# Performance work log

Hardware: AMD Instinct MI355X
Metric: run time of the kernel (lower is better)

## Reference

```python
import jax, jax.numpy as jnp
import numpy as np
import math

N_CELLS = 16384
INPUT_DIM = 512
HIDDEN = 512


def build_neighbors(n):
    n_bits = max(1, int(math.ceil(math.log2(n))))
    idx = np.arange(n)
    flips = [idx ^ (1 << b) for b in range(n_bits)]
    ring = [(idx + 1) % n, (idx - 1) % n]
    allnb = np.stack(flips + ring, axis=1)
    # dedupe per row; for power-of-2 n every row has exactly n_bits+1 uniques
    rows = [sorted(set(r.tolist())) for r in allnb]
    return np.asarray(rows, dtype=np.int32)


def setup_inputs() -> dict:
    key = jax.random.key(0)
    ks = jax.random.split(key, 12)
    n, d, h = N_CELLS, INPUT_DIM, HIDDEN
    amp = jax.random.uniform(ks[0], (n, h)) * 0.5 + 0.5
    phase = jax.random.normal(ks[1], (n, h)) * 0.3 + (2 * math.pi * jnp.arange(n) / n)[:, None]
    return {
        "x": jax.random.normal(ks[2], (1, d), dtype=jnp.float32),
        "pump_W": jax.random.normal(ks[3], (n, d), dtype=jnp.float32) / np.sqrt(d),
        "pump_b": jax.random.normal(ks[4], (n,), dtype=jnp.float32) * 0.01,
        "dec_W": jax.random.normal(ks[5], (d, 2 * h), dtype=jnp.float32) / np.sqrt(2 * h),
        "dec_b": jax.random.normal(ks[6], (d,), dtype=jnp.float32) * 0.01,
        "cs_re": (amp * jnp.cos(phase)).astype(jnp.float32),
        "cs_im": (amp * jnp.sin(phase)).astype(jnp.float32),
        "excited": jax.random.uniform(ks[7], (n,)) * 0.6,  # some cells above 0.5 threshold
        "phase_vel": jax.random.normal(ks[8], (n, h), dtype=jnp.float32) * 0.05,
        "cav_re": jax.random.normal(ks[9], (h,), dtype=jnp.float32) * 0.01,
        "cav_im": jax.random.normal(ks[10], (h,), dtype=jnp.float32) * 0.01,
        "neighbors": jnp.asarray(build_neighbors(n)),
    }


def reference(x, pump_W, pump_b, dec_W, dec_b, cs_re, cs_im, excited, phase_vel, cav_re, cav_im, neighbors):
    states = (cs_re + 1j * cs_im).astype(jnp.complex64)          # [n,h]
    cavity = (cav_re + 1j * cav_im).astype(jnp.complex64)        # [h]

    # pump + excited fraction update
    pump = jax.nn.sigmoid(x @ pump_W.T + pump_b)[0]              # [n]
    excited = jnp.clip(excited * 0.95 + pump * 0.05, 0.0, 1.0)

    # free phase rotation: polar(1, 0.1*phase_vel)
    states = states * jnp.exp(1j * (phase_vel * 0.1)).astype(jnp.complex64)

    # neighbor phase coupling (hypercube + ring, k=15 neighbors each)
    ang = jnp.angle(states)                                      # [n,h]
    nb_states = states[neighbors]                                # [n,k,h]
    coupling = jnp.cos(ang[:, None, :] - ang[neighbors])         # [n,k,h]
    interference = 0.1 * jnp.sum(coupling * nb_states, axis=1)   # [n,h]
    k = neighbors.shape[1]
    new_states = 0.7 * states + 0.3 * interference / k

    # lasing: population inversion threshold
    lasing = excited > 0.5                                       # [n]
    n_lasing = jnp.sum(lasing)
    maskf = lasing.astype(jnp.float32)[:, None]
    # emission uses pre-phase-lock states (torch copies lasing_cells first)
    emission = jnp.sum(new_states * maskf, axis=0) / jnp.maximum(n_lasing, 1).astype(jnp.float32)
    cavity_new = jnp.where(n_lasing > 0, 0.8 * cavity + 0.2 * emission, cavity)

    # phase-lock lasing cells to (old) cavity phase
    cavity_phase = jnp.angle(cavity)                             # old cavity
    new_ang = jnp.angle(new_states)
    locked = 0.3 * cavity_phase[None, :] + 0.7 * new_ang
    locked_states = jnp.abs(new_states) * jnp.exp(1j * locked)
    new_states = jnp.where(lasing[:, None], locked_states.astype(jnp.complex64), new_states)
    excited = jnp.where(lasing, excited * 0.9, excited * 0.98)

    # cavity feedback (updated cavity) + amplitude renorm
    new_states = new_states + 0.05 * cavity_new[None, :]
    amp = jnp.abs(new_states)
    amp = amp / (jnp.max(amp, axis=-1, keepdims=True) + 1e-8)
    final_states = (amp * jnp.exp(1j * jnp.angle(new_states))).astype(jnp.complex64)

    # decode cavity mode
    out_real = jnp.concatenate([cavity_new.real, cavity_new.imag])[None, :].astype(jnp.float32)  # [1,2h]
    pred = out_real @ dec_W.T + dec_b                            # [1, input_dim]
    tension = jnp.var(jnp.abs(final_states))
    return pred, tension
```

## Files before the change

kernel.cpp:

```cpp
#include <hip/hip_runtime.h>
#include <math.h>

#define N_CELLS 16384
#define HID 512
#define IND 512
#define KNB 15
#define NCOPY 64

#define ROT_BLOCKS  8192
#define PUMP_BLOCKS 4096
#define ZERO_BLOCKS 64

#define EMIS_OFF  128
#define LAS_OFF   (EMIS_OFF + NCOPY*1024*4)
#define CAV_OFF   (LAS_OFF + N_CELLS*4)
#define VPART_OFF (CAV_OFF + 1536*4)
#define ROT_OFF   (1<<20)
#define NST_OFF   (ROT_OFF + (size_t)N_CELLS*HID*8)

__global__ __launch_bounds__(256) void k_front(const float* __restrict__ cr,
                                               const float* __restrict__ ci,
                                               const float* __restrict__ pv,
                                               float2* __restrict__ rot,
                                               const float* __restrict__ x,
                                               const float* __restrict__ pW,
                                               const float* __restrict__ pb,
                                               const float* __restrict__ excited,
                                               int* __restrict__ lasing,
                                               float* __restrict__ emis) {
    int b = blockIdx.x;
    int tid = threadIdx.x;
    if (b < ROT_BLOCKS) {
        int i = b * 256 + tid;
        const float4* cr4 = (const float4*)cr;
        const float4* ci4 = (const float4*)ci;
        const float4* pv4 = (const float4*)pv;
        float4 a = cr4[i], bb = ci4[i], t = pv4[i];
        float s0, c0, s1, c1, s2, c2, s3, c3;
        __sincosf(0.1f * t.x, &s0, &c0);
        __sincosf(0.1f * t.y, &s1, &c1);
        __sincosf(0.1f * t.z, &s2, &c2);
        __sincosf(0.1f * t.w, &s3, &c3);
        float4 o0 = make_float4(a.x * c0 - bb.x * s0, a.x * s0 + bb.x * c0,
                                a.y * c1 - bb.y * s1, a.y * s1 + bb.y * c1);
        float4 o1 = make_float4(a.z * c2 - bb.z * s2, a.z * s2 + bb.z * c2,
                                a.w * c3 - bb.w * s3, a.w * s3 + bb.w * c3);
        float4* r4 = (float4*)rot;
        r4[2 * i]     = o0;
        r4[2 * i + 1] = o1;
    } else if (b < ROT_BLOCKS + PUMP_BLOCKS) {
        int gtid = (b - ROT_BLOCKS) * 256 + tid;
        int cell = gtid >> 6;
        int lane = gtid & 63;
        const float4* w4 = (const float4*)(pW + (size_t)cell * IND);
        const float4* x4 = (const float4*)x;
        float acc = 0.f;
#pragma unroll
        for (int t = 0; t < (IND / 4) / 64; ++t) {
            float4 a = w4[lane + 64 * t];
            float4 bx = x4[lane + 64 * t];
            acc += a.x * bx.x + a.y * bx.y + a.z * bx.z + a.w * bx.w;
        }
#pragma unroll
        for (int o = 32; o; o >>= 1) acc += __shfl_xor(acc, o, 64);
        if (lane == 0) {
            float p = 1.f / (1.f + expf(-(acc + pb[cell])));
            float e = excited[cell] * 0.95f + p * 0.05f;
            e = fminf(fmaxf(e, 0.f), 1.f);
            lasing[cell] = (e > 0.5f) ? 1 : 0;
        }
    } else {
        int idx = (b - ROT_BLOCKS - PUMP_BLOCKS) * 256 + tid;
        ((float4*)emis)[idx] = make_float4(0.f, 0.f, 0.f, 0.f);
    }
}

__global__ __launch_bounds__(256) void k_coup(const float2* __restrict__ rot,
                                              const int* __restrict__ nbrs,
                                              const int* __restrict__ lasing,
                                              float2* __restrict__ nst,
                                              float* __restrict__ emis) {
    __shared__ int nb[KNB];
    __shared__ int las;
    int cell = blockIdx.x;
    int tid = threadIdx.x;
    if (tid < KNB) nb[tid] = nbrs[cell * KNB + tid];
    if (tid == KNB) las = lasing[cell];
    __syncthreads();

    const float4* s4 = (const float4*)(rot + (size_t)cell * HID) + tid;
    float4 sa = *s4;
    float r0 = rsqrtf(sa.x * sa.x + sa.y * sa.y);
    float r1 = rsqrtf(sa.z * sa.z + sa.w * sa.w);

    float ar0 = 0.f, ai0 = 0.f, ar1 = 0.f, ai1 = 0.f;
#pragma unroll
    for (int t = 0; t < KNB; ++t) {
        const float4* q4 = (const float4*)(rot + (size_t)nb[t] * HID) + tid;
        float4 qa = *q4;
        float d, qi, w;
        d = sa.x * qa.x + sa.y * qa.y; qi = rsqrtf(qa.x * qa.x + qa.y * qa.y);
        w = d * r0 * qi; ar0 = fmaf(w, qa.x, ar0); ai0 = fmaf(w, qa.y, ai0);
        d = sa.z * qa.z + sa.w * qa.w; qi = rsqrtf(qa.z * qa.z + qa.w * qa.w);
        w = d * r1 * qi; ar1 = fmaf(w, qa.z, ar1); ai1 = fmaf(w, qa.w, ai1);
    }
    float4 oa = make_float4(0.7f * sa.x + 0.002f * ar0, 0.7f * sa.y + 0.002f * ai0,
                            0.7f * sa.z + 0.002f * ar1, 0.7f * sa.w + 0.002f * ai1);
    ((float4*)(nst + (size_t)cell * HID))[tid] = oa;
    if (las) {
        int c0 = tid << 1;
        float* em = emis + (size_t)(cell & (NCOPY - 1)) * 1024;
        atomicAdd(em + c0,     oa.x); atomicAdd(em + 512 + c0,     oa.y);
        atomicAdd(em + c0 + 1, oa.z); atomicAdd(em + 512 + c0 + 1, oa.w);
    }
}

__global__ __launch_bounds__(512) void k_cav(const float* __restrict__ emis,
                                             const int* __restrict__ lasv,
                                             const float* __restrict__ cavr,
                                             const float* __restrict__ cavi,
                                             float* __restrict__ cav) {
    __shared__ int cnt[8];
    __shared__ int snl;
    int c = threadIdx.x;
    int wid = c >> 6, lane = c & 63;
    const int4* l4 = (const int4*)lasv;
    int n = 0;
#pragma unroll
    for (int k = 0; k < N_CELLS / 4 / 512; ++k) {
        int4 v = l4[c + 512 * k];
        n += v.x + v.y + v.z + v.w;
    }
#pragma unroll
    for (int o = 32; o; o >>= 1) n += __shfl_xor(n, o, 64);
    if (lane == 0) cnt[wid] = n;
    __syncthreads();
    if (c == 0) { int t = 0; for (int k = 0; k < 8; ++k) t += cnt[k]; snl = t; }
    __syncthreads();
    int nl = snl;

    float er = 0.f, ei = 0.f;
#pragma unroll 8
    for (int k = 0; k < NCOPY; ++k) {
        er += emis[k * 1024 + c];
        ei += emis[k * 1024 + 512 + c];
    }
    float cr = cavr[c], ci = cavi[c];
    float nr, ni;
    if (nl > 0) {
        float inv = 1.f / (float)(nl > 1 ? nl : 1);
        nr = 0.8f * cr + 0.2f * er * inv;
        ni = 0.8f * ci + 0.2f * ei * inv;
    } else {
        nr = cr;
        ni = ci;
    }
    cav[c] = nr;
    cav[512 + c] = ni;
    cav[1024 + c] = atan2f(ci, cr);
}

__global__ __launch_bounds__(512) void k_pred(const float* __restrict__ cav,
                                              const float* __restrict__ dW,
                                              const float* __restrict__ db,
                                              float* __restrict__ out) {
    int gtid = blockIdx.x * 512 + threadIdx.x;
    int j = gtid >> 6;
    int lane = gtid & 63;
    const float4* w4 = (const float4*)(dW + (size_t)j * (2 * HID));
    const float4* o4 = (const float4*)cav;
    float acc = 0.f;
#pragma unroll
    for (int t = 0; t < (2 * HID / 4) / 64; ++t) {
        float4 a = w4[lane + 64 * t];
        float4 b = o4[lane + 64 * t];
        acc += a.x * b.x + a.y * b.y + a.z * b.z + a.w * b.w;
    }
#pragma unroll
    for (int o = 32; o; o >>= 1) acc += __shfl_xor(acc, o, 64);
    if (lane == 0) out[j] = acc + db[j];
}

__global__ __launch_bounds__(512) void k_fin(const float2* __restrict__ nst,
                                             const int* __restrict__ lasing,
                                             const float* __restrict__ cav,
                                             float2* __restrict__ vpart) {
    __shared__ float sred[8];
    __shared__ float sbc;
    int cell = blockIdx.x;
    int c = threadIdx.x;
    int wid = c >> 6, lane = c & 63;
    int las = lasing[cell];

    float2 v = nst[(size_t)cell * HID + c];
    if (las) {
        float r = sqrtf(v.x * v.x + v.y * v.y);
        float ang = atan2f(v.y, v.x);
        float locked = 0.3f * cav[1024 + c] + 0.7f * ang;
        float sn, cs;
        __sincosf(locked, &sn, &cs);
        v = make_float2(r * cs, r * sn);
    }
    v.x += 0.05f * cav[c];
    v.y += 0.05f * cav[512 + c];
    float amp = sqrtf(v.x * v.x + v.y * v.y);

    float m = amp;
#pragma unroll
    for (int o = 32; o; o >>= 1) m = fmaxf(m, __shfl_xor(m, o, 64));
    if (lane == 0) sred[wid] = m;
    __syncthreads();
    if (c == 0) {
        float mm = sred[0];
        for (int k = 1; k < 8; ++k) mm = fmaxf(mm, sred[k]);
        sbc = mm;
    }
    __syncthreads();
    float a = amp / (sbc + 1e-8f);

    float s1 = a, s2 = a * a;
#pragma unroll
    for (int o = 32; o; o >>= 1) { s1 += __shfl_xor(s1, o, 64); s2 += __shfl_xor(s2, o, 64); }
    __shared__ float w1[8], w2[8];
    if (lane == 0) { w1[wid] = s1; w2[wid] = s2; }
    __syncthreads();
    if (c == 0) {
        float t1 = 0.f, t2 = 0.f;
        for (int k = 0; k < 8; ++k) { t1 += w1[k]; t2 += w2[k]; }
        vpart[cell] = make_float2(t1, t2);
    }
}

__global__ __launch_bounds__(1024) void k_var(const float2* __restrict__ vpart,
                                              float* __restrict__ out) {
    __shared__ double l1[16], l2[16];
    int c = threadIdx.x;
    int wid = c >> 6, lane = c & 63;
    double s1 = 0.0, s2 = 0.0;
#pragma unroll
    for (int t = 0; t < N_CELLS / 1024; ++t) {
        float2 p = vpart[c + 1024 * t];
        s1 += (double)p.x;
        s2 += (double)p.y;
    }
#pragma unroll
    for (int o = 32; o; o >>= 1) { s1 += __shfl_xor(s1, o, 64); s2 += __shfl_xor(s2, o, 64); }
    if (lane == 0) { l1[wid] = s1; l2[wid] = s2; }
    __syncthreads();
    if (c == 0) {
        double t1 = 0.0, t2 = 0.0;
        for (int k = 0; k < 16; ++k) { t1 += l1[k]; t2 += l2[k]; }
        double n = (double)N_CELLS * (double)HID;
        double mean = t1 / n;
        out[IND] = (float)(t2 / n - mean * mean);
    }
}

extern "C" void kernel_launch(void* const* d_in, const int* in_sizes, int n_in,
                              void* d_out, int out_size, void* d_ws, size_t ws_size,
                              hipStream_t stream) {
    const float* x       = (const float*)d_in[0];
    const float* pump_W  = (const float*)d_in[1];
    const float* pump_b  = (const float*)d_in[2];
    const float* dec_W   = (const float*)d_in[3];
    const float* dec_b   = (const float*)d_in[4];
    const float* cs_re   = (const float*)d_in[5];
    const float* cs_im   = (const float*)d_in[6];
    const float* excited = (const float*)d_in[7];
    const float* pvel    = (const float*)d_in[8];
    const float* cav_re  = (const float*)d_in[9];
    const float* cav_im  = (const float*)d_in[10];
    const int*   nbrs    = (const int*)d_in[11];

    float* out = (float*)d_out;
    char* ws = (char*)d_ws;
    float*  emis  = (float*)(ws + EMIS_OFF);
    int*    lasv  = (int*)(ws + LAS_OFF);
    float*  cav   = (float*)(ws + CAV_OFF);
    float2* vpart = (float2*)(ws + VPART_OFF);
    float2* rot   = (float2*)(ws + ROT_OFF);
    float2* nst   = (float2*)(ws + NST_OFF);

    k_front<<<ROT_BLOCKS + PUMP_BLOCKS + ZERO_BLOCKS, 256, 0, stream>>>(
        cs_re, cs_im, pvel, rot, x, pump_W, pump_b, excited, lasv, emis);
    k_coup<<<N_CELLS, 256, 0, stream>>>(rot, nbrs, lasv, nst, emis);
    k_cav<<<1, 512, 0, stream>>>(emis, lasv, cav_re, cav_im, cav);
    k_pred<<<64, 512, 0, stream>>>(cav, dec_W, dec_b, out);
    k_fin<<<N_CELLS, 512, 0, stream>>>(nst, lasv, cav, vpart);
    k_var<<<1, 1024, 0, stream>>>(vpart, out);
}
```

Before: 307.9 us.

## Store rotated and coupled states in fp16 and compute coupling with packed half math

The rotated state buffer and the post-coupling state buffer are now stored as half2 instead of float2, which halves their memory footprint and the traffic for the 15-neighbour gather in k_coup. The neighbour coupling inner loop now runs in packed fp16 arithmetic (hfma2 and h2rsqrt), and the self-normalisation factor is applied once after the loop. In exchange the states lose precision and accumulation is done in fp16, which may exceed tolerance. k_fin reads the half2 buffer and converts it back to float.

After: 268.4 us. 1.15x faster.

```diff
diff --git a/kernel.cpp b/kernel.cpp
--- a/kernel.cpp
+++ b/kernel.cpp
@@ -1,4 +1,5 @@
 #include <hip/hip_runtime.h>
+#include <hip/hip_fp16.h>
 #include <math.h>
 
 #define N_CELLS 16384
@@ -16,12 +17,15 @@
 #define CAV_OFF   (LAS_OFF + N_CELLS*4)
 #define VPART_OFF (CAV_OFF + 1536*4)
 #define ROT_OFF   (1<<20)
-#define NST_OFF   (ROT_OFF + (size_t)N_CELLS*HID*8)
+#define NST_OFF   (ROT_OFF + (size_t)N_CELLS*HID*4)
+
+__device__ inline __half2 f2h2(float f) { union { float f; __half2 h; } u; u.f = f; return u.h; }
+__device__ inline float   h22f(__half2 h) { union { float f; __half2 h; } u; u.h = h; return u.f; }
 
 __global__ __launch_bounds__(256) void k_front(const float* __restrict__ cr,
                                                const float* __restrict__ ci,
                                                const float* __restrict__ pv,
-                                               float2* __restrict__ rot,
+                                               __half2* __restrict__ rot,
                                                const float* __restrict__ x,
                                                const float* __restrict__ pW,
                                                const float* __restrict__ pb,
@@ -41,13 +45,11 @@
         __sincosf(0.1f * t.y, &s1, &c1);
         __sincosf(0.1f * t.z, &s2, &c2);
         __sincosf(0.1f * t.w, &s3, &c3);
-        float4 o0 = make_float4(a.x * c0 - bb.x * s0, a.x * s0 + bb.x * c0,
-                                a.y * c1 - bb.y * s1, a.y * s1 + bb.y * c1);
-        float4 o1 = make_float4(a.z * c2 - bb.z * s2, a.z * s2 + bb.z * c2,
-                                a.w * c3 - bb.w * s3, a.w * s3 + bb.w * c3);
-        float4* r4 = (float4*)rot;
-        r4[2 * i]     = o0;
-        r4[2 * i + 1] = o1;
+        __half2 p0 = __floats2half2_rn(a.x * c0 - bb.x * s0, a.x * s0 + bb.x * c0);
+        __half2 p1 = __floats2half2_rn(a.y * c1 - bb.y * s1, a.y * s1 + bb.y * c1);
+        __half2 p2 = __floats2half2_rn(a.z * c2 - bb.z * s2, a.z * s2 + bb.z * c2);
+        __half2 p3 = __floats2half2_rn(a.w * c3 - bb.w * s3, a.w * s3 + bb.w * c3);
+        ((float4*)rot)[i] = make_float4(h22f(p0), h22f(p1), h22f(p2), h22f(p3));
     } else if (b < ROT_BLOCKS + PUMP_BLOCKS) {
         int gtid = (b - ROT_BLOCKS) * 256 + tid;
         int cell = gtid >> 6;
@@ -75,10 +77,10 @@
     }
 }
 
-__global__ __launch_bounds__(256) void k_coup(const float2* __restrict__ rot,
+__global__ __launch_bounds__(256) void k_coup(const __half2* __restrict__ rot,
                                               const int* __restrict__ nbrs,
                                               const int* __restrict__ lasing,
-                                              float2* __restrict__ nst,
+                                              __half2* __restrict__ nst,
                                               float* __restrict__ emis) {
     __shared__ int nb[KNB];
     __shared__ int las;
@@ -88,30 +90,42 @@
     if (tid == KNB) las = lasing[cell];
     __syncthreads();
 
-    const float4* s4 = (const float4*)(rot + (size_t)cell * HID) + tid;
-    float4 sa = *s4;
-    float r0 = rsqrtf(sa.x * sa.x + sa.y * sa.y);
-    float r1 = rsqrtf(sa.z * sa.z + sa.w * sa.w);
-
-    float ar0 = 0.f, ai0 = 0.f, ar1 = 0.f, ai1 = 0.f;
+    const float2* rot2 = (const float2*)rot;
+    float2 raw = rot2[(size_t)cell * (HID / 2) + tid];
+    __half2 sa = f2h2(raw.x), sb = f2h2(raw.y);
+    __half2 sre = __halves2half2(__low2half(sa), __low2half(sb));
+    __half2 sim = __halves2half2(__high2half(sa), __high2half(sb));
+    float s0x = __low2float(sa), s0y = __high2float(sa);
+    float s1x = __low2float(sb), s1y = __high2float(sb);
+    float r0 = rsqrtf(s0x * s0x + s0y * s0y);
+    float r1 = rsqrtf(s1x * s1x + s1y * s1y);
+
+    __half2 are = __float2half2_rn(0.f), aim = __float2half2_rn(0.f);
 #pragma unroll
     for (int t = 0; t < KNB; ++t) {
-        const float4* q4 = (const float4*)(rot + (size_t)nb[t] * HID) + tid;
-        float4 qa = *q4;
-        float d, qi, w;
-        d = sa.x * qa.x + sa.y * qa.y; qi = rsqrtf(qa.x * qa.x + qa.y * qa.y);
-        w = d * r0 * qi; ar0 = fmaf(w, qa.x, ar0); ai0 = fmaf(w, qa.y, ai0);
-        d = sa.z * qa.z + sa.w * qa.w; qi = rsqrtf(qa.z * qa.z + qa.w * qa.w);
-        w = d * r1 * qi; ar1 = fmaf(w, qa.z, ar1); ai1 = fmaf(w, qa.w, ai1);
-    }
-    float4 oa = make_float4(0.7f * sa.x + 0.002f * ar0, 0.7f * sa.y + 0.002f * ai0,
-                            0.7f * sa.z + 0.002f * ar1, 0.7f * sa.w + 0.002f * ai1);
-    ((float4*)(nst + (size_t)cell * HID))[tid] = oa;
+        float2 qraw = rot2[(size_t)nb[t] * (HID / 2) + tid];
+        __half2 qa = f2h2(qraw.x), qb = f2h2(qraw.y);
+        __half2 qre = __halves2half2(__low2half(qa), __low2half(qb));
+        __half2 qim = __halves2half2(__high2half(qa), __high2half(qb));
+        __half2 d  = __hfma2(sim, qim, __hmul2(sre, qre));
+        __half2 qn = __hfma2(qim, qim, __hmul2(qre, qre));
+        __half2 t2 = __hmul2(d, h2rsqrt(qn));
+        are = __hfma2(t2, qre, are);
+        aim = __hfma2(t2, qim, aim);
+    }
+    float ar0 = __low2float(are), ar1 = __high2float(are);
+    float ai0 = __low2float(aim), ai1 = __high2float(aim);
+    float k0 = 0.002f * r0, k1 = 0.002f * r1;
+    float nr0 = 0.7f * s0x + k0 * ar0, ni0 = 0.7f * s0y + k0 * ai0;
+    float nr1 = 0.7f * s1x + k1 * ar1, ni1 = 0.7f * s1y + k1 * ai1;
+    float2 st = make_float2(h22f(__floats2half2_rn(nr0, ni0)),
+                            h22f(__floats2half2_rn(nr1, ni1)));
+    ((float2*)nst)[(size_t)cell * (HID / 2) + tid] = st;
     if (las) {
         int c0 = tid << 1;
         float* em = emis + (size_t)(cell & (NCOPY - 1)) * 1024;
-        atomicAdd(em + c0,     oa.x); atomicAdd(em + 512 + c0,     oa.y);
-        atomicAdd(em + c0 + 1, oa.z); atomicAdd(em + 512 + c0 + 1, oa.w);
+        atomicAdd(em + c0,     nr0); atomicAdd(em + 512 + c0,     ni0);
+        atomicAdd(em + c0 + 1, nr1); atomicAdd(em + 512 + c0 + 1, ni1);
     }
 }
 
@@ -181,7 +195,7 @@
     if (lane == 0) out[j] = acc + db[j];
 }
 
-__global__ __launch_bounds__(512) void k_fin(const float2* __restrict__ nst,
+__global__ __launch_bounds__(512) void k_fin(const __half2* __restrict__ nst,
                                              const int* __restrict__ lasing,
                                              const float* __restrict__ cav,
                                              float2* __restrict__ vpart) {
@@ -192,18 +206,19 @@
     int wid = c >> 6, lane = c & 63;
     int las = lasing[cell];
 
-    float2 v = nst[(size_t)cell * HID + c];
+    __half2 vh = nst[(size_t)cell * HID + c];
+    float vx = __low2float(vh), vy = __high2float(vh);
     if (las) {
-        float r = sqrtf(v.x * v.x + v.y * v.y);
-        float ang = atan2f(v.y, v.x);
+        float r = sqrtf(vx * vx + vy * vy);
+        float ang = atan2f(vy, vx);
         float locked = 0.3f * cav[1024 + c] + 0.7f * ang;
         float sn, cs;
         __sincosf(locked, &sn, &cs);
-        v = make_float2(r * cs, r * sn);
-    }
-    v.x += 0.05f * cav[c];
-    v.y += 0.05f * cav[512 + c];
-    float amp = sqrtf(v.x * v.x + v.y * v.y);
+        vx = r * cs; vy = r * sn;
+    }
+    vx += 0.05f * cav[c];
+    vy += 0.05f * cav[512 + c];
+    float amp = sqrtf(vx * vx + vy * vy);
 
     float m = amp;
 #pragma unroll
@@ -274,12 +289,12 @@
 
     float* out = (float*)d_out;
     char* ws = (char*)d_ws;
-    float*  emis  = (float*)(ws + EMIS_OFF);
-    int*    lasv  = (int*)(ws + LAS_OFF);
-    float*  cav   = (float*)(ws + CAV_OFF);
-    float2* vpart = (float2*)(ws + VPART_OFF);
-    float2* rot   = (float2*)(ws + ROT_OFF);
-    float2* nst   = (float2*)(ws + NST_OFF);
+    float*   emis  = (float*)(ws + EMIS_OFF);
+    int*     lasv  = (int*)(ws + LAS_OFF);
+    float*   cav   = (float*)(ws + CAV_OFF);
+    float2*  vpart = (float2*)(ws + VPART_OFF);
+    __half2* rot   = (__half2*)(ws + ROT_OFF);
+    __half2* nst   = (__half2*)(ws + NST_OFF);
 
     k_front<<<ROT_BLOCKS + PUMP_BLOCKS + ZERO_BLOCKS, 256, 0, stream>>>(
         cs_re, cs_im, pvel, rot, x, pump_W, pump_b, excited, lasv, emis);
```
